# Optimization experiments

Hardware: AMD Instinct MI355X
Metric: run time of the kernel (lower is better)

Reference implementation:

```python
import jax, jax.numpy as jnp
import numpy as np

B, S, D, H = 4, 2048, 512, 8
HD = D // H  # 64


def setup_inputs() -> dict:
    key = jax.random.key(0)
    ks = jax.random.split(key, 7)
    scale = 1.0 / np.sqrt(D)
    return {
        "query": jax.random.normal(ks[0], (B, S, D), jnp.float32),
        "key": jax.random.normal(ks[1], (B, S, D), jnp.float32),
        "value": jax.random.normal(ks[2], (B, S, D), jnp.float32),
        # Only the `query` Linear and fc_out are actually used in the original forward
        "Wq": jax.random.uniform(ks[3], (D, D), jnp.float32, -scale, scale),
        "bq": jnp.zeros((D,), jnp.float32),
        "Wo": jax.random.uniform(ks[4], (D, D), jnp.float32, -scale, scale),
        "bo": jnp.zeros((D,), jnp.float32),
    }


def reference(query, key, value, Wq, bq, Wo, bo):
    # Faithful to source: Q, K, V all use the *query* projection (bug preserved)
    def proj(x):
        # [B,S,D] -> [B,H,S,HD]
        y = x @ Wq + bq
        return y.reshape(B, S, H, HD).transpose(0, 2, 1, 3)

    Q, K, V = proj(query), proj(key), proj(value)
    scores = jnp.einsum("bhqd,bhkd->bhqk", Q, K) / jnp.sqrt(jnp.float32(HD))
    attn = jax.nn.softmax(scores, axis=-1)
    x = jnp.einsum("bhqk,bhkd->bhqd", attn, V)
    x = x.transpose(0, 2, 1, 3).reshape(B, S, D)
    return x @ Wo + bo
```

## Files before the change

### kernel.cpp

```cpp
#include <hip/hip_runtime.h>
#include <math.h>

#define B_ 4
#define S_ 2048
#define D_ 512
#define H_ 8
#define HD_ 64
#define SZ_ (B_ * S_ * D_)
#define WSZ_ (D_ * D_)
#define BSH_ (B_ * S_ * H_)

#define QSCALE_ 0.18033688011112042f

typedef _Float16 v4h __attribute__((ext_vector_type(4)));
typedef _Float16 v8h __attribute__((ext_vector_type(8)));
typedef float    v4f __attribute__((ext_vector_type(4)));

__global__ __launch_bounds__(256) void wtrans_kernel(const float* __restrict__ Wq,
                                                     const float* __restrict__ Wo,
                                                     _Float16* __restrict__ Wt) {
    __shared__ float Ts[64][65];
    const float* W = blockIdx.z ? Wo : Wq;
    _Float16* dst = Wt + (size_t)blockIdx.z * WSZ_;
    const int t = threadIdx.x;
    const int k0 = blockIdx.y * 64, n0 = blockIdx.x * 64;
#pragma unroll
    for (int i = 0; i < 4; i++) {
        int c = t + i * 256;
        int kk = c >> 4, nc = (c & 15) * 4;
        float4 w = *(const float4*)&W[(size_t)(k0 + kk) * 512 + n0 + nc];
        Ts[nc + 0][kk] = w.x;
        Ts[nc + 1][kk] = w.y;
        Ts[nc + 2][kk] = w.z;
        Ts[nc + 3][kk] = w.w;
    }
    __syncthreads();
#pragma unroll
    for (int i = 0; i < 2; i++) {
        int c = t + i * 256;
        int n = c >> 3, kc = (c & 7) * 8;
        v8h p;
#pragma unroll
        for (int j = 0; j < 8; j++) p[j] = (_Float16)Ts[n][kc + j];
        *(v8h*)&dst[(size_t)(n0 + n) * 512 + k0 + kc] = p;
    }
}

__global__ __launch_bounds__(256) void proj_mfma(const float* __restrict__ q,
                                                 const float* __restrict__ k,
                                                 const float* __restrict__ v,
                                                 const _Float16* __restrict__ Wt,
                                                 const float* __restrict__ bq,
                                                 _Float16* __restrict__ Qh,
                                                 _Float16* __restrict__ Kh,
                                                 _Float16* __restrict__ VT) {
    __shared__ _Float16 As[128 * 72];
    __shared__ _Float16 Bs[128 * 72];
    const int z  = blockIdx.z;
    const float* X = (z == 0) ? q : ((z == 1) ? k : v);
    const int n0 = blockIdx.x * 128, m0 = blockIdx.y * 128;
    const int t    = threadIdx.x;
    const int lane = t & 63;
    const int w    = t >> 6;
    const int wm   = w >> 1, wn = w & 1;
    const int quad = lane >> 4, l16 = lane & 15;

    v4f acc[4][4];
#pragma unroll
    for (int mi = 0; mi < 4; mi++)
#pragma unroll
        for (int ni = 0; ni < 4; ni++) acc[mi][ni] = (v4f)0.f;

    int rr[4], cc[4];
    const float*    Ap[4];
    const _Float16* Bp[4];
#pragma unroll
    for (int i = 0; i < 4; i++) {
        int s = t + i * 256;
        rr[i] = s >> 3;
        cc[i] = (s & 7) * 8;
        Ap[i] = X + (size_t)(m0 + rr[i]) * 512 + cc[i];
        Bp[i] = Wt + (size_t)(n0 + rr[i]) * 512 + cc[i];
    }

    v4f pa[4][2];
    v8h pb[4];
#pragma unroll
    for (int i = 0; i < 4; i++) {
        pa[i][0] = *(const v4f*)(Ap[i] + 0);
        pa[i][1] = *(const v4f*)(Ap[i] + 4);
        pb[i]    = *(const v8h*)(Bp[i] + 0);
    }

    for (int k0 = 0; k0 < 512; k0 += 64) {
        v8h af4[4];
#pragma unroll
        for (int i = 0; i < 4; i++)
            af4[i] = __builtin_shufflevector(__builtin_convertvector(pa[i][0], v4h),
                                             __builtin_convertvector(pa[i][1], v4h),
                                             0, 1, 2, 3, 4, 5, 6, 7);
        __syncthreads();
#pragma unroll
        for (int i = 0; i < 4; i++) {
            *(v8h*)&As[rr[i] * 72 + cc[i]] = af4[i];
            *(v8h*)&Bs[rr[i] * 72 + cc[i]] = pb[i];
        }
        __syncthreads();

        if (k0 + 64 < 512) {
#pragma unroll
            for (int i = 0; i < 4; i++) {
                pa[i][0] = *(const v4f*)(Ap[i] + k0 + 64);
                pa[i][1] = *(const v4f*)(Ap[i] + k0 + 68);
                pb[i]    = *(const v8h*)(Bp[i] + k0 + 64);
            }
        }

#pragma unroll
        for (int ks = 0; ks < 2; ks++) {
            v8h af[4], bf[4];
#pragma unroll
            for (int mi = 0; mi < 4; mi++)
                af[mi] = *(const v8h*)&As[(wm * 64 + mi * 16 + l16) * 72 + ks * 32 + quad * 8];
#pragma unroll
            for (int ni = 0; ni < 4; ni++)
                bf[ni] = *(const v8h*)&Bs[(wn * 64 + ni * 16 + l16) * 72 + ks * 32 + quad * 8];
#pragma unroll
            for (int mi = 0; mi < 4; mi++)
#pragma unroll
                for (int ni = 0; ni < 4; ni++)
                    acc[mi][ni] = __builtin_amdgcn_mfma_f32_16x16x32_f16(af[mi], bf[ni], acc[mi][ni], 0, 0, 0);
        }
    }

    if (z < 2) {
        _Float16* Y = z ? Kh : Qh;
        const float sc = z ? 1.f : QSCALE_;
#pragma unroll
        for (int mi = 0; mi < 4; mi++) {
            int mb = m0 + wm * 64 + mi * 16 + quad * 4;
#pragma unroll
            for (int ni = 0; ni < 4; ni++) {
                int n = n0 + wn * 64 + ni * 16 + l16;
                float bj = bq[n];
#pragma unroll
                for (int r = 0; r < 4; r++)
                    Y[(size_t)(mb + r) * 512 + n] = (_Float16)((acc[mi][ni][r] + bj) * sc);
            }
        }
    } else {
#pragma unroll
        for (int mi = 0; mi < 4; mi++) {
            int tile0 = (m0 & 2047) + wm * 64;
            int pos = tile0 + (mi >> 1) * 32 + quad * 8 + (mi & 1) * 4;
            int b = m0 >> 11;
#pragma unroll
            for (int ni = 0; ni < 4; ni++) {
                int n = n0 + wn * 64 + ni * 16 + l16;
                int h = n >> 6, d = n & 63;
                float bj = bq[n];
                v4h pk;
#pragma unroll
                for (int r = 0; r < 4; r++) pk[r] = (_Float16)(acc[mi][ni][r] + bj);
                *(v4h*)&VT[(((size_t)b * H_ + h) * HD_ + d) * S_ + pos] = pk;
            }
        }
    }
}

__global__ __launch_bounds__(256) void outproj_mfma(const float* __restrict__ Op,
                                                    const float* __restrict__ lp,
                                                    const _Float16* __restrict__ Wt,
                                                    const float* __restrict__ bo,
                                                    float* __restrict__ out) {
    __shared__ _Float16 As[64 * 40];
    __shared__ _Float16 Bs[128 * 40];
    const int n0 = blockIdx.x * 128, m0 = blockIdx.y * 64;
    const int t    = threadIdx.x;
    const int lane = t & 63;
    const int w    = t >> 6;
    const int wm   = w >> 1, wn = w & 1;
    const int quad = lane >> 4, l16 = lane & 15;

    v4f acc[2][4];
#pragma unroll
    for (int mi = 0; mi < 2; mi++)
#pragma unroll
        for (int ni = 0; ni < 4; ni++) acc[mi][ni] = (v4f)0.f;

    const int ra = t >> 2,  ca = (t & 3) * 8;
    const int rb0 = t >> 2, cb0 = (t & 3) * 8;
    const int rb1 = (t + 256) >> 2, cb1 = (t & 3) * 8;
    const float* O1p = Op + (size_t)(m0 + ra) * 512 + ca;
    const float* O2p = O1p + SZ_;
    const float* lpp = lp + (size_t)(m0 + ra) * H_;
    const _Float16* B0 = Wt + (size_t)WSZ_ + (size_t)(n0 + rb0) * 512 + cb0;
    const _Float16* B1 = Wt + (size_t)WSZ_ + (size_t)(n0 + rb1) * 512 + cb1;

    v4f a0 = *(const v4f*)(O1p + 0), a1 = *(const v4f*)(O1p + 4);
    v4f c0 = *(const v4f*)(O2p + 0), c1 = *(const v4f*)(O2p + 4);
    float lv = lpp[0] + lpp[BSH_];
    v8h b0 = *(const v8h*)(B0 + 0), b1 = *(const v8h*)(B1 + 0);

    for (int k0 = 0; k0 < 512; k0 += 32) {
        float linv = __builtin_amdgcn_rcpf(lv);
        v4f sa = (a0 + c0) * linv, sb = (a1 + c1) * linv;
        v8h af0 = __builtin_shufflevector(__builtin_convertvector(sa, v4h),
                                          __builtin_convertvector(sb, v4h),
                                          0, 1, 2, 3, 4, 5, 6, 7);
        __syncthreads();
        *(v8h*)&As[ra * 40 + ca] = af0;
        *(v8h*)&Bs[rb0 * 40 + cb0] = b0;
        *(v8h*)&Bs[rb1 * 40 + cb1] = b1;
        __syncthreads();

        if (k0 + 32 < 512) {
            int kn = k0 + 32;
            int hh = (kn + ca) >> 6;
            a0 = *(const v4f*)(O1p + kn); a1 = *(const v4f*)(O1p + kn + 4);
            c0 = *(const v4f*)(O2p + kn); c1 = *(const v4f*)(O2p + kn + 4);
            lv = lpp[hh] + lpp[BSH_ + hh];
            b0 = *(const v8h*)(B0 + kn);
            b1 = *(const v8h*)(B1 + kn);
        }

        v8h af[2], bf[4];
#pragma unroll
        for (int mi = 0; mi < 2; mi++)
            af[mi] = *(const v8h*)&As[(wm * 32 + mi * 16 + l16) * 40 + quad * 8];
#pragma unroll
        for (int ni = 0; ni < 4; ni++)
            bf[ni] = *(const v8h*)&Bs[(wn * 64 + ni * 16 + l16) * 40 + quad * 8];
#pragma unroll
        for (int mi = 0; mi < 2; mi++)
#pragma unroll
            for (int ni = 0; ni < 4; ni++)
                acc[mi][ni] = __builtin_amdgcn_mfma_f32_16x16x32_f16(af[mi], bf[ni], acc[mi][ni], 0, 0, 0);
    }

#pragma unroll
    for (int mi = 0; mi < 2; mi++) {
        int mb = m0 + wm * 32 + mi * 16 + quad * 4;
#pragma unroll
        for (int ni = 0; ni < 4; ni++) {
            int n = n0 + wn * 64 + ni * 16 + l16;
            float bj = bo[n];
#pragma unroll
            for (int r = 0; r < 4; r++)
                out[(size_t)(mb + r) * 512 + n] = acc[mi][ni][r] + bj;
        }
    }
}

__global__ __launch_bounds__(256) void flash_attn_f16(const _Float16* __restrict__ Qh,
                                                      const _Float16* __restrict__ Kh,
                                                      const _Float16* __restrict__ VT,
                                                      float* __restrict__ Op,
                                                      float* __restrict__ lp) {
    __shared__ _Float16 Ks[128 * 72];
    __shared__ _Float16 Vs[64 * 136];

    const int t     = threadIdx.x;
    const int lane  = t & 63;
    const int w     = t >> 6;
    const int quad  = lane >> 4;
    const int l16   = lane & 15;
    const int q0    = blockIdx.x * 128;
    const int h     = blockIdx.y;
    const int b     = blockIdx.z >> 1;
    const int split = blockIdx.z & 1;

    const size_t base  = (size_t)b * S_ * D_ + (size_t)h * HD_;
    const size_t vbase = ((size_t)b * H_ + h) * HD_ * (size_t)S_;

    v8h qf[2][2];
#pragma unroll
    for (int nb = 0; nb < 2; nb++) {
        const _Float16* qrow = Qh + base + (size_t)(q0 + w * 32 + nb * 16 + l16) * D_;
        qf[nb][0] = *(const v8h*)(qrow + quad * 8);
        qf[nb][1] = *(const v8h*)(qrow + 32 + quad * 8);
    }

    v4f o[2][4];
#pragma unroll
    for (int nb = 0; nb < 2; nb++)
#pragma unroll
        for (int i = 0; i < 4; i++) o[nb][i] = (v4f)0.f;
    float l_lane[2] = {0.f, 0.f};

    const int kbeg = split * (S_ / 2);
    const int kend = kbeg + S_ / 2;

    v8h kv[4], vv[4];
#define LOADKV(kk)                                                             \
    do {                                                                       \
        _Pragma("unroll") for (int i = 0; i < 4; i++) {                        \
            int c = t + i * 256;                                               \
            kv[i] = *(const v8h*)(Kh + base + (size_t)((kk) + (c >> 3)) * D_ + (c & 7) * 8); \
            vv[i] = *(const v8h*)(VT + vbase + (size_t)(c >> 4) * S_ + (kk) + (c & 15) * 8); \
        }                                                                      \
    } while (0)

    LOADKV(kbeg);

    for (int kk0 = kbeg; kk0 < kend; kk0 += 128) {
        __syncthreads();
#pragma unroll
        for (int i = 0; i < 4; i++) {
            int c = t + i * 256;
            *(v8h*)&Ks[(c >> 3) * 72 + (c & 7) * 8] = kv[i];
            *(v8h*)&Vs[(c >> 4) * 136 + (c & 15) * 8] = vv[i];
        }
        __syncthreads();

        if (kk0 + 128 < kend) LOADKV(kk0 + 128);

#pragma unroll
        for (int hh = 0; hh < 2; hh++) {
            v4f sc[4][2];
#pragma unroll
            for (int mb = 0; mb < 4; mb++)
#pragma unroll
                for (int nb = 0; nb < 2; nb++) sc[mb][nb] = (v4f)0.f;
#pragma unroll
            for (int ks = 0; ks < 2; ks++) {
#pragma unroll
                for (int mb = 0; mb < 4; mb++) {
                    v8h ak = *(const v8h*)&Ks[(hh * 64 + mb * 16 + l16) * 72 + ks * 32 + quad * 8];
#pragma unroll
                    for (int nb = 0; nb < 2; nb++)
                        sc[mb][nb] = __builtin_amdgcn_mfma_f32_16x16x32_f16(ak, qf[nb][ks], sc[mb][nb], 0, 0, 0);
                }
            }

            v4h pf[4][2];
#pragma unroll
            for (int nb = 0; nb < 2; nb++) {
#pragma unroll
                for (int mb = 0; mb < 4; mb++) {
                    v4f pv;
#pragma unroll
                    for (int r = 0; r < 4; r++) pv[r] = __builtin_amdgcn_exp2f(sc[mb][nb][r]);
                    pf[mb][nb] = __builtin_convertvector(pv, v4h);
                    l_lane[nb] += (pv[0] + pv[1]) + (pv[2] + pv[3]);
                }
            }

#pragma unroll
            for (int p = 0; p < 2; p++) {
#pragma unroll
                for (int dblk = 0; dblk < 4; dblk++) {
                    v8h vf2 = *(const v8h*)&Vs[(dblk * 16 + l16) * 136 + hh * 64 + p * 32 + quad * 8];
                    v4h vlo = __builtin_shufflevector(vf2, vf2, 0, 1, 2, 3);
                    v4h vhi = __builtin_shufflevector(vf2, vf2, 4, 5, 6, 7);
#pragma unroll
                    for (int nb = 0; nb < 2; nb++) {
                        o[nb][dblk] = __builtin_amdgcn_mfma_f32_16x16x16f16(vlo, pf[2 * p][nb], o[nb][dblk], 0, 0, 0);
                        o[nb][dblk] = __builtin_amdgcn_mfma_f32_16x16x16f16(vhi, pf[2 * p + 1][nb], o[nb][dblk], 0, 0, 0);
                    }
                }
            }
        }
    }
#undef LOADKV

    float* Ops = Op + (size_t)split * SZ_;
#pragma unroll
    for (int nb = 0; nb < 2; nb++) {
        float rs = l_lane[nb];
        rs += __shfl_xor(rs, 16);
        rs += __shfl_xor(rs, 32);
        int qrow = q0 + w * 32 + nb * 16 + l16;
        if (quad == 0)
            lp[(size_t)split * BSH_ + ((size_t)b * S_ + qrow) * H_ + h] = rs;
        const size_t rbase = base + (size_t)qrow * D_;
#pragma unroll
        for (int dblk = 0; dblk < 4; dblk++)
            *(v4f*)&Ops[rbase + dblk * 16 + quad * 4] = o[nb][dblk];
    }
}

extern "C" void kernel_launch(void* const* d_in, const int* in_sizes, int n_in,
                              void* d_out, int out_size, void* d_ws, size_t ws_size,
                              hipStream_t stream) {
    const float* query = (const float*)d_in[0];
    const float* key   = (const float*)d_in[1];
    const float* value = (const float*)d_in[2];
    const float* Wq    = (const float*)d_in[3];
    const float* bq    = (const float*)d_in[4];
    const float* Wo    = (const float*)d_in[5];
    const float* bo    = (const float*)d_in[6];
    float* out = (float*)d_out;

    _Float16* ws = (_Float16*)d_ws;
    _Float16* Qh = ws;
    _Float16* Kh = ws + (size_t)SZ_;
    _Float16* VT = ws + 2 * (size_t)SZ_;
    _Float16* Wt = ws + 3 * (size_t)SZ_;
    float*    Op = (float*)(ws + 3 * (size_t)SZ_ + 2 * (size_t)WSZ_);
    float*    lp = Op + 2 * (size_t)SZ_;

    wtrans_kernel<<<dim3(8, 8, 2), 256, 0, stream>>>(Wq, Wo, Wt);
    proj_mfma<<<dim3(4, 64, 3), 256, 0, stream>>>(query, key, value, Wt, bq, Qh, Kh, VT);
    flash_attn_f16<<<dim3(S_ / 128, H_, B_ * 2), 256, 0, stream>>>(Qh, Kh, VT, Op, lp);
    outproj_mfma<<<dim3(4, 128, 1), 256, 0, stream>>>(Op, lp, Wt, bo, out);
}
```

Before: 200.6 us.

## Pre-tile weights into swizzled blocks and stream them via global_load_lds

```diff
diff --git a/kernel.cpp b/kernel.cpp
--- a/kernel.cpp
+++ b/kernel.cpp
@@ -16,38 +16,42 @@
 typedef _Float16 v8h __attribute__((ext_vector_type(8)));
 typedef float    v4f __attribute__((ext_vector_type(4)));
 
+__device__ __forceinline__ void gload16(const void* g, void* l) {
+    __builtin_amdgcn_global_load_lds((__attribute__((address_space(1))) void*)g,
+                                     (__attribute__((address_space(3))) void*)l,
+                                     16, 0, 0);
+}
+
 __global__ __launch_bounds__(256) void wtrans_kernel(const float* __restrict__ Wq,
                                                      const float* __restrict__ Wo,
                                                      _Float16* __restrict__ Wt) {
-    __shared__ float Ts[64][65];
-    const float* W = blockIdx.z ? Wo : Wq;
-    _Float16* dst = Wt + (size_t)blockIdx.z * WSZ_;
+    __shared__ float Ts[64][132];
+    const int kc = blockIdx.x, nt = blockIdx.y, mat = blockIdx.z;
+    const float* W = mat ? Wo : Wq;
+    const int k0 = kc * 64, n0 = nt * 128;
     const int t = threadIdx.x;
-    const int k0 = blockIdx.y * 64, n0 = blockIdx.x * 64;
+#pragma unroll
+    for (int i = 0; i < 8; i++) {
+        int s2 = t + i * 256;
+        int kk = s2 >> 5, nc = (s2 & 31) * 4;
+        *(float4*)&Ts[kk][nc] = *(const float4*)&W[(size_t)(k0 + kk) * 512 + n0 + nc];
+    }
+    __syncthreads();
+    _Float16* blk = Wt + (((size_t)mat * 4 + nt) * 8 + kc) * 8192;
 #pragma unroll
     for (int i = 0; i < 4; i++) {
-        int c = t + i * 256;
-        int kk = c >> 4, nc = (c & 15) * 4;
-        float4 w = *(const float4*)&W[(size_t)(k0 + kk) * 512 + n0 + nc];
-        Ts[nc + 0][kk] = w.x;
-        Ts[nc + 1][kk] = w.y;
-        Ts[nc + 2][kk] = w.z;
-        Ts[nc + 3][kk] = w.w;
-    }
-    __syncthreads();
-#pragma unroll
-    for (int i = 0; i < 2; i++) {
-        int c = t + i * 256;
-        int n = c >> 3, kc = (c & 7) * 8;
+        int s2 = t + i * 256;
+        int r = s2 >> 3, s = s2 & 7;
+        int kl = (s ^ (r & 7)) * 8;
         v8h p;
 #pragma unroll
-        for (int j = 0; j < 8; j++) p[j] = (_Float16)Ts[n][kc + j];
-        *(v8h*)&dst[(size_t)(n0 + n) * 512 + k0 + kc] = p;
+        for (int j = 0; j < 8; j++) p[j] = (_Float16)Ts[kl + j][r];
+        *(v8h*)&blk[r * 64 + s * 8] = p;
     }
 }
 
 __global__ __launch_bounds__(256) void proj_mfma(const float* __restrict__ q,
-                                                 const float* __restrict__ k,
+                                                 const float* __restrict__ kin,
                                                  const float* __restrict__ v,
                                                  const _Float16* __restrict__ Wt,
                                                  const float* __restrict__ bq,
@@ -55,15 +59,20 @@
                                                  _Float16* __restrict__ Kh,
                                                  _Float16* __restrict__ VT) {
     __shared__ _Float16 As[128 * 72];
-    __shared__ _Float16 Bs[128 * 72];
-    const int z  = blockIdx.z;
-    const float* X = (z == 0) ? q : ((z == 1) ? k : v);
-    const int n0 = blockIdx.x * 128, m0 = blockIdx.y * 128;
+    __shared__ _Float16 Bs[128 * 64];
+    const int d   = blockIdx.x;
+    const int wl  = (d & 7) * 96 + (d >> 3);
+    const int z   = wl >> 8;
+    const int rem = wl & 255;
+    const int m0  = (rem >> 2) * 128;
+    const int n_t = rem & 3, n0 = n_t * 128;
+    const float* X = (z == 0) ? q : ((z == 1) ? kin : v);
     const int t    = threadIdx.x;
     const int lane = t & 63;
     const int w    = t >> 6;
     const int wm   = w >> 1, wn = w & 1;
     const int quad = lane >> 4, l16 = lane & 15;
+    const _Float16* WtB = Wt + (size_t)n_t * 8 * 8192;
 
     v4f acc[4][4];
 #pragma unroll
@@ -72,24 +81,20 @@
         for (int ni = 0; ni < 4; ni++) acc[mi][ni] = (v4f)0.f;
 
     int rr[4], cc[4];
-    const float*    Ap[4];
-    const _Float16* Bp[4];
+    const float* Ap[4];
 #pragma unroll
     for (int i = 0; i < 4; i++) {
         int s = t + i * 256;
         rr[i] = s >> 3;
         cc[i] = (s & 7) * 8;
         Ap[i] = X + (size_t)(m0 + rr[i]) * 512 + cc[i];
-        Bp[i] = Wt + (size_t)(n0 + rr[i]) * 512 + cc[i];
     }
 
     v4f pa[4][2];
-    v8h pb[4];
 #pragma unroll
     for (int i = 0; i < 4; i++) {
         pa[i][0] = *(const v4f*)(Ap[i] + 0);
         pa[i][1] = *(const v4f*)(Ap[i] + 4);
-        pb[i]    = *(const v8h*)(Bp[i] + 0);
     }
 
     for (int k0 = 0; k0 < 512; k0 += 64) {
@@ -100,11 +105,16 @@
                                              __builtin_convertvector(pa[i][1], v4h),
                                              0, 1, 2, 3, 4, 5, 6, 7);
         __syncthreads();
-#pragma unroll
-        for (int i = 0; i < 4; i++) {
+
+        {
+            const _Float16* wsrc = WtB + (size_t)(k0 >> 6) * 8192 + w * 2048 + lane * 8;
+            _Float16* ldst = &Bs[w * 2048];
+#pragma unroll
+            for (int i = 0; i < 4; i++) gload16(wsrc + i * 512, ldst + i * 512);
+        }
+#pragma unroll
+        for (int i = 0; i < 4; i++)
             *(v8h*)&As[rr[i] * 72 + cc[i]] = af4[i];
-            *(v8h*)&Bs[rr[i] * 72 + cc[i]] = pb[i];
-        }
         __syncthreads();
 
         if (k0 + 64 < 512) {
@@ -112,7 +122,6 @@
             for (int i = 0; i < 4; i++) {
                 pa[i][0] = *(const v4f*)(Ap[i] + k0 + 64);
                 pa[i][1] = *(const v4f*)(Ap[i] + k0 + 68);
-                pb[i]    = *(const v8h*)(Bp[i] + k0 + 64);
             }
         }
 
@@ -123,8 +132,10 @@
             for (int mi = 0; mi < 4; mi++)
                 af[mi] = *(const v8h*)&As[(wm * 64 + mi * 16 + l16) * 72 + ks * 32 + quad * 8];
 #pragma unroll
-            for (int ni = 0; ni < 4; ni++)
-                bf[ni] = *(const v8h*)&Bs[(wn * 64 + ni * 16 + l16) * 72 + ks * 32 + quad * 8];
+            for (int ni = 0; ni < 4; ni++) {
+                int row = wn * 64 + ni * 16 + l16;
+                bf[ni] = *(const v8h*)&Bs[row * 64 + ((ks * 32 + quad * 8) ^ ((row & 7) * 8))];
+            }
 #pragma unroll
             for (int mi = 0; mi < 4; mi++)
 #pragma unroll
@@ -157,12 +168,12 @@
 #pragma unroll
             for (int ni = 0; ni < 4; ni++) {
                 int n = n0 + wn * 64 + ni * 16 + l16;
-                int h = n >> 6, d = n & 63;
+                int h = n >> 6, dd = n & 63;
                 float bj = bq[n];
                 v4h pk;
 #pragma unroll
                 for (int r = 0; r < 4; r++) pk[r] = (_Float16)(acc[mi][ni][r] + bj);
-                *(v4h*)&VT[(((size_t)b * H_ + h) * HD_ + d) * S_ + pos] = pk;
+                *(v4h*)&VT[(((size_t)b * H_ + h) * HD_ + dd) * S_ + pos] = pk;
             }
         }
     }
@@ -173,14 +184,18 @@
                                                     const _Float16* __restrict__ Wt,
                                                     const float* __restrict__ bo,
                                                     float* __restrict__ out) {
-    __shared__ _Float16 As[64 * 40];
-    __shared__ _Float16 Bs[128 * 40];
-    const int n0 = blockIdx.x * 128, m0 = blockIdx.y * 64;
+    __shared__ _Float16 As[64 * 72];
+    __shared__ _Float16 Bs[128 * 64];
+    const int d   = blockIdx.x;
+    const int wl  = (d & 7) * 64 + (d >> 3);
+    const int n_t = wl & 3, n0 = n_t * 128;
+    const int m0  = (wl >> 2) * 64;
     const int t    = threadIdx.x;
     const int lane = t & 63;
     const int w    = t >> 6;
     const int wm   = w >> 1, wn = w & 1;
     const int quad = lane >> 4, l16 = lane & 15;
+    const _Float16* WtB = Wt + (size_t)(4 + n_t) * 8 * 8192;
 
     v4f acc[2][4];
 #pragma unroll
@@ -188,54 +203,84 @@
 #pragma unroll
         for (int ni = 0; ni < 4; ni++) acc[mi][ni] = (v4f)0.f;
 
-    const int ra = t >> 2,  ca = (t & 3) * 8;
-    const int rb0 = t >> 2, cb0 = (t & 3) * 8;
-    const int rb1 = (t + 256) >> 2, cb1 = (t & 3) * 8;
-    const float* O1p = Op + (size_t)(m0 + ra) * 512 + ca;
-    const float* O2p = O1p + SZ_;
-    const float* lpp = lp + (size_t)(m0 + ra) * H_;
-    const _Float16* B0 = Wt + (size_t)WSZ_ + (size_t)(n0 + rb0) * 512 + cb0;
-    const _Float16* B1 = Wt + (size_t)WSZ_ + (size_t)(n0 + rb1) * 512 + cb1;
-
-    v4f a0 = *(const v4f*)(O1p + 0), a1 = *(const v4f*)(O1p + 4);
-    v4f c0 = *(const v4f*)(O2p + 0), c1 = *(const v4f*)(O2p + 4);
-    float lv = lpp[0] + lpp[BSH_];
-    v8h b0 = *(const v8h*)(B0 + 0), b1 = *(const v8h*)(B1 + 0);
-
-    for (int k0 = 0; k0 < 512; k0 += 32) {
-        float linv = __builtin_amdgcn_rcpf(lv);
-        v4f sa = (a0 + c0) * linv, sb = (a1 + c1) * linv;
-        v8h af0 = __builtin_shufflevector(__builtin_convertvector(sa, v4h),
-                                          __builtin_convertvector(sb, v4h),
-                                          0, 1, 2, 3, 4, 5, 6, 7);
-        __syncthreads();
-        *(v8h*)&As[ra * 40 + ca] = af0;
-        *(v8h*)&Bs[rb0 * 40 + cb0] = b0;
-        *(v8h*)&Bs[rb1 * 40 + cb1] = b1;
-        __syncthreads();
-
-        if (k0 + 32 < 512) {
-            int kn = k0 + 32;
-            int hh = (kn + ca) >> 6;
-            a0 = *(const v4f*)(O1p + kn); a1 = *(const v4f*)(O1p + kn + 4);
-            c0 = *(const v4f*)(O2p + kn); c1 = *(const v4f*)(O2p + kn + 4);
-            lv = lpp[hh] + lpp[BSH_ + hh];
-            b0 = *(const v8h*)(B0 + kn);
-            b1 = *(const v8h*)(B1 + kn);
-        }
-
-        v8h af[2], bf[4];
-#pragma unroll
-        for (int mi = 0; mi < 2; mi++)
-            af[mi] = *(const v8h*)&As[(wm * 32 + mi * 16 + l16) * 40 + quad * 8];
-#pragma unroll
-        for (int ni = 0; ni < 4; ni++)
-            bf[ni] = *(const v8h*)&Bs[(wn * 64 + ni * 16 + l16) * 40 + quad * 8];
-#pragma unroll
-        for (int mi = 0; mi < 2; mi++)
-#pragma unroll
-            for (int ni = 0; ni < 4; ni++)
-                acc[mi][ni] = __builtin_amdgcn_mfma_f32_16x16x32_f16(af[mi], bf[ni], acc[mi][ni], 0, 0, 0);
+    int rw[2], cw[2];
+    const float* O1p[2];
+    const float* O2p[2];
+    const float* lpp[2];
+#pragma unroll
+    for (int i = 0; i < 2; i++) {
+        int s2 = t + i * 256;
+        rw[i] = s2 >> 3;
+        cw[i] = (s2 & 7) * 8;
+        O1p[i] = Op + (size_t)(m0 + rw[i]) * 512 + cw[i];
+        O2p[i] = O1p[i] + SZ_;
+        lpp[i] = lp + (size_t)(m0 + rw[i]) * H_;
+    }
+
+    v4f pa0[2], pa1[2], pc0[2], pc1[2];
+    float lvv[2];
+#pragma unroll
+    for (int i = 0; i < 2; i++) {
+        pa0[i] = *(const v4f*)(O1p[i] + 0);
+        pa1[i] = *(const v4f*)(O1p[i] + 4);
+        pc0[i] = *(const v4f*)(O2p[i] + 0);
+        pc1[i] = *(const v4f*)(O2p[i] + 4);
+        lvv[i] = lpp[i][0] + lpp[i][BSH_];
+    }
+
+    for (int k0 = 0; k0 < 512; k0 += 64) {
+        v8h af16[2];
+#pragma unroll
+        for (int i = 0; i < 2; i++) {
+            float linv = __builtin_amdgcn_rcpf(lvv[i]);
+            v4f sa = (pa0[i] + pc0[i]) * linv;
+            v4f sb = (pa1[i] + pc1[i]) * linv;
+            af16[i] = __builtin_shufflevector(__builtin_convertvector(sa, v4h),
+                                              __builtin_convertvector(sb, v4h),
+                                              0, 1, 2, 3, 4, 5, 6, 7);
+        }
+        __syncthreads();
+
+        {
+            const _Float16* wsrc = WtB + (size_t)(k0 >> 6) * 8192 + w * 2048 + lane * 8;
+            _Float16* ldst = &Bs[w * 2048];
+#pragma unroll
+            for (int i = 0; i < 4; i++) gload16(wsrc + i * 512, ldst + i * 512);
+        }
+#pragma unroll
+        for (int i = 0; i < 2; i++)
+            *(v8h*)&As[rw[i] * 72 + cw[i]] = af16[i];
+        __syncthreads();
+
+        if (k0 + 64 < 512) {
+            int kn = k0 + 64, hh = kn >> 6;
+#pragma unroll
+            for (int i = 0; i < 2; i++) {
+                pa0[i] = *(const v4f*)(O1p[i] + kn);
+                pa1[i] = *(const v4f*)(O1p[i] + kn + 4);
+                pc0[i] = *(const v4f*)(O2p[i] + kn);
+                pc1[i] = *(const v4f*)(O2p[i] + kn + 4);
+                lvv[i] = lpp[i][hh] + lpp[i][BSH_ + hh];
+            }
+        }
+
+#pragma unroll
+        for (int ks = 0; ks < 2; ks++) {
+            v8h af[2], bf[4];
+#pragma unroll
+            for (int mi = 0; mi < 2; mi++)
+                af[mi] = *(const v8h*)&As[(wm * 32 + mi * 16 + l16) * 72 + ks * 32 + quad * 8];
+#pragma unroll
+            for (int ni = 0; ni < 4; ni++) {
+                int row = wn * 64 + ni * 16 + l16;
+                bf[ni] = *(const v8h*)&Bs[row * 64 + ((ks * 32 + quad * 8) ^ ((row & 7) * 8))];
+            }
+#pragma unroll
+            for (int mi = 0; mi < 2; mi++)
+#pragma unroll
+                for (int ni = 0; ni < 4; ni++)
+                    acc[mi][ni] = __builtin_amdgcn_mfma_f32_16x16x32_f16(af[mi], bf[ni], acc[mi][ni], 0, 0, 0);
+        }
     }
 
 #pragma unroll
@@ -400,8 +445,8 @@
     float*    Op = (float*)(ws + 3 * (size_t)SZ_ + 2 * (size_t)WSZ_);
     float*    lp = Op + 2 * (size_t)SZ_;
 
-    wtrans_kernel<<<dim3(8, 8, 2), 256, 0, stream>>>(Wq, Wo, Wt);
-    proj_mfma<<<dim3(4, 64, 3), 256, 0, stream>>>(query, key, value, Wt, bq, Qh, Kh, VT);
+    wtrans_kernel<<<dim3(8, 4, 2), 256, 0, stream>>>(Wq, Wo, Wt);
+    proj_mfma<<<dim3(768), 256, 0, stream>>>(query, key, value, Wt, bq, Qh, Kh, VT);
     flash_attn_f16<<<dim3(S_ / 128, H_, B_ * 2), 256, 0, stream>>>(Qh, Kh, VT, Op, lp);
-    outproj_mfma<<<dim3(4, 128, 1), 256, 0, stream>>>(Op, lp, Wt, bo, out);
-}
+    outproj_mfma<<<dim3(512), 256, 0, stream>>>(Op, lp, Wt, bo, out);
+}
```

After: 197.3 us. About the same (-1.7%).

## Keep full weight slice in LDS and stream activations directly from global

Applied to the files above, without the earlier changes.

```diff
diff --git a/kernel.cpp b/kernel.cpp
--- a/kernel.cpp
+++ b/kernel.cpp
@@ -16,153 +16,131 @@
 typedef _Float16 v8h __attribute__((ext_vector_type(8)));
 typedef float    v4f __attribute__((ext_vector_type(4)));
 
+__device__ __forceinline__ void gload16(const void* g, void* l) {
+    __builtin_amdgcn_global_load_lds((__attribute__((address_space(1))) void*)g,
+                                     (__attribute__((address_space(3))) void*)l,
+                                     16, 0, 0);
+}
+
+__device__ __forceinline__ v8h pack8(v4f a, v4f b) {
+    return __builtin_shufflevector(__builtin_convertvector(a, v4h),
+                                   __builtin_convertvector(b, v4h),
+                                   0, 1, 2, 3, 4, 5, 6, 7);
+}
+
 __global__ __launch_bounds__(256) void wtrans_kernel(const float* __restrict__ Wq,
                                                      const float* __restrict__ Wo,
                                                      _Float16* __restrict__ Wt) {
-    __shared__ float Ts[64][65];
-    const float* W = blockIdx.z ? Wo : Wq;
-    _Float16* dst = Wt + (size_t)blockIdx.z * WSZ_;
+    __shared__ float Ts[64][68];
+    const int kc = blockIdx.x, nt = blockIdx.y, mat = blockIdx.z;
+    const float* W = mat ? Wo : Wq;
+    const int k0 = kc * 64, n0 = nt * 64;
     const int t = threadIdx.x;
-    const int k0 = blockIdx.y * 64, n0 = blockIdx.x * 64;
 #pragma unroll
     for (int i = 0; i < 4; i++) {
-        int c = t + i * 256;
-        int kk = c >> 4, nc = (c & 15) * 4;
-        float4 w = *(const float4*)&W[(size_t)(k0 + kk) * 512 + n0 + nc];
-        Ts[nc + 0][kk] = w.x;
-        Ts[nc + 1][kk] = w.y;
-        Ts[nc + 2][kk] = w.z;
-        Ts[nc + 3][kk] = w.w;
+        int s2 = t + i * 256;
+        int kk = s2 >> 4, nc = (s2 & 15) * 4;
+        *(float4*)&Ts[kk][nc] = *(const float4*)&W[(size_t)(k0 + kk) * 512 + n0 + nc];
     }
     __syncthreads();
+    _Float16* blk = Wt + (((size_t)mat * 8 + nt) * 8 + kc) * 4096;
 #pragma unroll
     for (int i = 0; i < 2; i++) {
-        int c = t + i * 256;
-        int n = c >> 3, kc = (c & 7) * 8;
+        int s2 = t + i * 256;
+        int r = s2 >> 3, s = s2 & 7;
+        int kl = (s ^ (r & 7)) * 8;
         v8h p;
 #pragma unroll
-        for (int j = 0; j < 8; j++) p[j] = (_Float16)Ts[n][kc + j];
-        *(v8h*)&dst[(size_t)(n0 + n) * 512 + k0 + kc] = p;
+        for (int j = 0; j < 8; j++) p[j] = (_Float16)Ts[kl + j][r];
+        *(v8h*)&blk[r * 64 + s * 8] = p;
     }
 }
 
 __global__ __launch_bounds__(256) void proj_mfma(const float* __restrict__ q,
-                                                 const float* __restrict__ k,
+                                                 const float* __restrict__ kin,
                                                  const float* __restrict__ v,
                                                  const _Float16* __restrict__ Wt,
                                                  const float* __restrict__ bq,
                                                  _Float16* __restrict__ Qh,
                                                  _Float16* __restrict__ Kh,
                                                  _Float16* __restrict__ VT) {
-    __shared__ _Float16 As[128 * 72];
-    __shared__ _Float16 Bs[128 * 72];
-    const int z  = blockIdx.z;
-    const float* X = (z == 0) ? q : ((z == 1) ? k : v);
-    const int n0 = blockIdx.x * 128, m0 = blockIdx.y * 128;
-    const int t    = threadIdx.x;
-    const int lane = t & 63;
-    const int w    = t >> 6;
-    const int wm   = w >> 1, wn = w & 1;
+    __shared__ __align__(16) _Float16 Bs[32768];
+    const int dblk = blockIdx.x;
+    const int xcd = dblk & 7, ii = dblk >> 3;
+    const int nt = ii & 7;
+    const int g  = ((ii >> 3) << 3) | xcd;
+    const int z  = g >> 5;
+    const int m0 = (g & 31) * 256;
+    const float* X = (z == 0) ? q : ((z == 1) ? kin : v);
+    const int t = threadIdx.x;
+    const int lane = t & 63, w = t >> 6;
     const int quad = lane >> 4, l16 = lane & 15;
 
-    v4f acc[4][4];
-#pragma unroll
-    for (int mi = 0; mi < 4; mi++)
-#pragma unroll
-        for (int ni = 0; ni < 4; ni++) acc[mi][ni] = (v4f)0.f;
-
-    int rr[4], cc[4];
-    const float*    Ap[4];
-    const _Float16* Bp[4];
-#pragma unroll
-    for (int i = 0; i < 4; i++) {
-        int s = t + i * 256;
-        rr[i] = s >> 3;
-        cc[i] = (s & 7) * 8;
-        Ap[i] = X + (size_t)(m0 + rr[i]) * 512 + cc[i];
-        Bp[i] = Wt + (size_t)(n0 + rr[i]) * 512 + cc[i];
-    }
-
-    v4f pa[4][2];
-    v8h pb[4];
-#pragma unroll
-    for (int i = 0; i < 4; i++) {
-        pa[i][0] = *(const v4f*)(Ap[i] + 0);
-        pa[i][1] = *(const v4f*)(Ap[i] + 4);
-        pb[i]    = *(const v8h*)(Bp[i] + 0);
-    }
-
-    for (int k0 = 0; k0 < 512; k0 += 64) {
-        v8h af4[4];
-#pragma unroll
-        for (int i = 0; i < 4; i++)
-            af4[i] = __builtin_shufflevector(__builtin_convertvector(pa[i][0], v4h),
-                                             __builtin_convertvector(pa[i][1], v4h),
-                                             0, 1, 2, 3, 4, 5, 6, 7);
-        __syncthreads();
-#pragma unroll
-        for (int i = 0; i < 4; i++) {
-            *(v8h*)&As[rr[i] * 72 + cc[i]] = af4[i];
-            *(v8h*)&Bs[rr[i] * 72 + cc[i]] = pb[i];
-        }
-        __syncthreads();
-
-        if (k0 + 64 < 512) {
-#pragma unroll
-            for (int i = 0; i < 4; i++) {
-                pa[i][0] = *(const v4f*)(Ap[i] + k0 + 64);
-                pa[i][1] = *(const v4f*)(Ap[i] + k0 + 68);
-                pb[i]    = *(const v8h*)(Bp[i] + k0 + 64);
-            }
-        }
-
-#pragma unroll
-        for (int ks = 0; ks < 2; ks++) {
-            v8h af[4], bf[4];
-#pragma unroll
-            for (int mi = 0; mi < 4; mi++)
-                af[mi] = *(const v8h*)&As[(wm * 64 + mi * 16 + l16) * 72 + ks * 32 + quad * 8];
-#pragma unroll
-            for (int ni = 0; ni < 4; ni++)
-                bf[ni] = *(const v8h*)&Bs[(wn * 64 + ni * 16 + l16) * 72 + ks * 32 + quad * 8];
-#pragma unroll
-            for (int mi = 0; mi < 4; mi++)
-#pragma unroll
-                for (int ni = 0; ni < 4; ni++)
-                    acc[mi][ni] = __builtin_amdgcn_mfma_f32_16x16x32_f16(af[mi], bf[ni], acc[mi][ni], 0, 0, 0);
-        }
-    }
-
-    if (z < 2) {
-        _Float16* Y = z ? Kh : Qh;
-        const float sc = z ? 1.f : QSCALE_;
-#pragma unroll
-        for (int mi = 0; mi < 4; mi++) {
-            int mb = m0 + wm * 64 + mi * 16 + quad * 4;
-#pragma unroll
-            for (int ni = 0; ni < 4; ni++) {
-                int n = n0 + wn * 64 + ni * 16 + l16;
-                float bj = bq[n];
-#pragma unroll
-                for (int r = 0; r < 4; r++)
-                    Y[(size_t)(mb + r) * 512 + n] = (_Float16)((acc[mi][ni][r] + bj) * sc);
-            }
-        }
-    } else {
-#pragma unroll
-        for (int mi = 0; mi < 4; mi++) {
-            int tile0 = (m0 & 2047) + wm * 64;
-            int pos = tile0 + (mi >> 1) * 32 + quad * 8 + (mi & 1) * 4;
-            int b = m0 >> 11;
-#pragma unroll
-            for (int ni = 0; ni < 4; ni++) {
-                int n = n0 + wn * 64 + ni * 16 + l16;
-                int h = n >> 6, d = n & 63;
-                float bj = bq[n];
-                v4h pk;
-#pragma unroll
-                for (int r = 0; r < 4; r++) pk[r] = (_Float16)(acc[mi][ni][r] + bj);
-                *(v4h*)&VT[(((size_t)b * H_ + h) * HD_ + d) * S_ + pos] = pk;
+    const _Float16* psrc = Wt + (size_t)nt * 32768 + ((size_t)w * 64 + lane) * 8;
+    _Float16* pdst = &Bs[(size_t)w * 512];
+#pragma unroll
+    for (int j = 0; j < 16; j++)
+        gload16(psrc + j * 2048, pdst + j * 2048);
+    __syncthreads();
+
+    for (int pass = 0; pass < 2; ++pass) {
+        const int r0 = m0 + pass * 128 + w * 32;
+        const float* A0 = X + (size_t)(r0 + l16) * 512 + quad * 8;
+        const float* A1 = A0 + 16 * 512;
+
+        v4f acc[2][4];
+#pragma unroll
+        for (int mi = 0; mi < 2; mi++)
+#pragma unroll
+            for (int ni = 0; ni < 4; ni++) acc[mi][ni] = (v4f)0.f;
+
+#pragma unroll
+        for (int kc = 0; kc < 8; ++kc) {
+#pragma unroll
+            for (int ks = 0; ks < 2; ++ks) {
+                const int ko = kc * 64 + ks * 32;
+                v8h af0 = pack8(*(const v4f*)(A0 + ko), *(const v4f*)(A0 + ko + 4));
+                v8h af1 = pack8(*(const v4f*)(A1 + ko), *(const v4f*)(A1 + ko + 4));
+                const int sx = ks * 32 + quad * 8;
+#pragma unroll
+                for (int ni = 0; ni < 4; ++ni) {
+                    const int rb = ni * 16 + l16;
+                    v8h bf = *(const v8h*)&Bs[kc * 4096 + rb * 64 + (sx ^ ((rb & 7) * 8))];
+                    acc[0][ni] = __builtin_amdgcn_mfma_f32_16x16x32_f16(af0, bf, acc[0][ni], 0, 0, 0);
+                    acc[1][ni] = __builtin_amdgcn_mfma_f32_16x16x32_f16(af1, bf, acc[1][ni], 0, 0, 0);
+                }
+            }
+        }
+
+        if (z < 2) {
+            _Float16* Y = z ? Kh : Qh;
+            const float sc = z ? 1.f : QSCALE_;
+#pragma unroll
+            for (int mi = 0; mi < 2; mi++) {
+                int mb = r0 + mi * 16 + quad * 4;
+#pragma unroll
+                for (int ni = 0; ni < 4; ni++) {
+                    int n = nt * 64 + ni * 16 + l16;
+                    float bj = bq[n];
+#pragma unroll
+                    for (int r = 0; r < 4; r++)
+                        Y[(size_t)(mb + r) * 512 + n] = (_Float16)((acc[mi][ni][r] + bj) * sc);
+                }
+            }
+        } else {
+            const int b = r0 >> 11;
+#pragma unroll
+            for (int mi = 0; mi < 2; mi++) {
+                int pos = (r0 & 2047) + quad * 8 + mi * 4;
+#pragma unroll
+                for (int ni = 0; ni < 4; ni++) {
+                    int n = nt * 64 + ni * 16 + l16;
+                    float bj = bq[n];
+                    v4h pk;
+#pragma unroll
+                    for (int r = 0; r < 4; r++) pk[r] = (_Float16)(acc[mi][ni][r] + bj);
+                    *(v4h*)&VT[(((size_t)b * H_ + nt) * HD_ + ni * 16 + l16) * S_ + pos] = pk;
+                }
             }
         }
     }
@@ -173,81 +151,78 @@
                                                     const _Float16* __restrict__ Wt,
                                                     const float* __restrict__ bo,
                                                     float* __restrict__ out) {
-    __shared__ _Float16 As[64 * 40];
-    __shared__ _Float16 Bs[128 * 40];
-    const int n0 = blockIdx.x * 128, m0 = blockIdx.y * 64;
-    const int t    = threadIdx.x;
-    const int lane = t & 63;
-    const int w    = t >> 6;
-    const int wm   = w >> 1, wn = w & 1;
+    __shared__ __align__(16) _Float16 Bs[32768];
+    const int dblk = blockIdx.x;
+    const int xcd = dblk & 7, ii = dblk >> 3;
+    const int nt = ii & 7;
+    const int mc = ((ii >> 3) << 3) | xcd;
+    const int m0 = mc * 256;
+    const int t = threadIdx.x;
+    const int lane = t & 63, w = t >> 6;
     const int quad = lane >> 4, l16 = lane & 15;
 
-    v4f acc[2][4];
-#pragma unroll
-    for (int mi = 0; mi < 2; mi++)
-#pragma unroll
-        for (int ni = 0; ni < 4; ni++) acc[mi][ni] = (v4f)0.f;
-
-    const int ra = t >> 2,  ca = (t & 3) * 8;
-    const int rb0 = t >> 2, cb0 = (t & 3) * 8;
-    const int rb1 = (t + 256) >> 2, cb1 = (t & 3) * 8;
-    const float* O1p = Op + (size_t)(m0 + ra) * 512 + ca;
-    const float* O2p = O1p + SZ_;
-    const float* lpp = lp + (size_t)(m0 + ra) * H_;
-    const _Float16* B0 = Wt + (size_t)WSZ_ + (size_t)(n0 + rb0) * 512 + cb0;
-    const _Float16* B1 = Wt + (size_t)WSZ_ + (size_t)(n0 + rb1) * 512 + cb1;
-
-    v4f a0 = *(const v4f*)(O1p + 0), a1 = *(const v4f*)(O1p + 4);
-    v4f c0 = *(const v4f*)(O2p + 0), c1 = *(const v4f*)(O2p + 4);
-    float lv = lpp[0] + lpp[BSH_];
-    v8h b0 = *(const v8h*)(B0 + 0), b1 = *(const v8h*)(B1 + 0);
-
-    for (int k0 = 0; k0 < 512; k0 += 32) {
-        float linv = __builtin_amdgcn_rcpf(lv);
-        v4f sa = (a0 + c0) * linv, sb = (a1 + c1) * linv;
-        v8h af0 = __builtin_shufflevector(__builtin_convertvector(sa, v4h),
-                                          __builtin_convertvector(sb, v4h),
-                                          0, 1, 2, 3, 4, 5, 6, 7);
-        __syncthreads();
-        *(v8h*)&As[ra * 40 + ca] = af0;
-        *(v8h*)&Bs[rb0 * 40 + cb0] = b0;
-        *(v8h*)&Bs[rb1 * 40 + cb1] = b1;
-        __syncthreads();
-
-        if (k0 + 32 < 512) {
-            int kn = k0 + 32;
-            int hh = (kn + ca) >> 6;
-            a0 = *(const v4f*)(O1p + kn); a1 = *(const v4f*)(O1p + kn + 4);
-            c0 = *(const v4f*)(O2p + kn); c1 = *(const v4f*)(O2p + kn + 4);
-            lv = lpp[hh] + lpp[BSH_ + hh];
-            b0 = *(const v8h*)(B0 + kn);
-            b1 = *(const v8h*)(B1 + kn);
-        }
-
-        v8h af[2], bf[4];
+    const _Float16* psrc = Wt + (size_t)(8 + nt) * 32768 + ((size_t)w * 64 + lane) * 8;
+    _Float16* pdst = &Bs[(size_t)w * 512];
+#pragma unroll
+    for (int j = 0; j < 16; j++)
+        gload16(psrc + j * 2048, pdst + j * 2048);
+    __syncthreads();
+
+    for (int pass = 0; pass < 2; ++pass) {
+        const int r0 = m0 + pass * 128 + w * 32;
+        const float* P0 = Op + (size_t)(r0 + l16) * 512 + quad * 8;
+        const float* P1 = P0 + 16 * 512;
+        const float* Q0 = P0 + SZ_;
+        const float* Q1 = P1 + SZ_;
+        const float* lp0 = lp + (size_t)(r0 + l16) * 8;
+        const float* lp1 = lp0 + 16 * 8;
+
+        float linv0[8], linv1[8];
+#pragma unroll
+        for (int kc = 0; kc < 8; kc++) {
+            linv0[kc] = __builtin_amdgcn_rcpf(lp0[kc] + lp0[BSH_ + kc]);
+            linv1[kc] = __builtin_amdgcn_rcpf(lp1[kc] + lp1[BSH_ + kc]);
+        }
+
+        v4f acc[2][4];
 #pragma unroll
         for (int mi = 0; mi < 2; mi++)
-            af[mi] = *(const v8h*)&As[(wm * 32 + mi * 16 + l16) * 40 + quad * 8];
-#pragma unroll
-        for (int ni = 0; ni < 4; ni++)
-            bf[ni] = *(const v8h*)&Bs[(wn * 64 + ni * 16 + l16) * 40 + quad * 8];
-#pragma unroll
-        for (int mi = 0; mi < 2; mi++)
-#pragma unroll
-            for (int ni = 0; ni < 4; ni++)
-                acc[mi][ni] = __builtin_amdgcn_mfma_f32_16x16x32_f16(af[mi], bf[ni], acc[mi][ni], 0, 0, 0);
-    }
-
-#pragma unroll
-    for (int mi = 0; mi < 2; mi++) {
-        int mb = m0 + wm * 32 + mi * 16 + quad * 4;
-#pragma unroll
-        for (int ni = 0; ni < 4; ni++) {
-            int n = n0 + wn * 64 + ni * 16 + l16;
-            float bj = bo[n];
-#pragma unroll
-            for (int r = 0; r < 4; r++)
-                out[(size_t)(mb + r) * 512 + n] = acc[mi][ni][r] + bj;
+#pragma unroll
+            for (int ni = 0; ni < 4; ni++) acc[mi][ni] = (v4f)0.f;
+
+#pragma unroll
+        for (int kc = 0; kc < 8; ++kc) {
+#pragma unroll
+            for (int ks = 0; ks < 2; ++ks) {
+                const int ko = kc * 64 + ks * 32;
+                v4f s00 = (*(const v4f*)(P0 + ko) + *(const v4f*)(Q0 + ko)) * linv0[kc];
+                v4f s01 = (*(const v4f*)(P0 + ko + 4) + *(const v4f*)(Q0 + ko + 4)) * linv0[kc];
+                v4f s10 = (*(const v4f*)(P1 + ko) + *(const v4f*)(Q1 + ko)) * linv1[kc];
+                v4f s11 = (*(const v4f*)(P1 + ko + 4) + *(const v4f*)(Q1 + ko + 4)) * linv1[kc];
+                v8h af0 = pack8(s00, s01);
+                v8h af1 = pack8(s10, s11);
+                const int sx = ks * 32 + quad * 8;
+#pragma unroll
+                for (int ni = 0; ni < 4; ++ni) {
+                    const int rb = ni * 16 + l16;
+                    v8h bf = *(const v8h*)&Bs[kc * 4096 + rb * 64 + (sx ^ ((rb & 7) * 8))];
+                    acc[0][ni] = __builtin_amdgcn_mfma_f32_16x16x32_f16(af0, bf, acc[0][ni], 0, 0, 0);
+                    acc[1][ni] = __builtin_amdgcn_mfma_f32_16x16x32_f16(af1, bf, acc[1][ni], 0, 0, 0);
+                }
+            }
+        }
+
+#pragma unroll
+        for (int mi = 0; mi < 2; mi++) {
+            int mb = r0 + mi * 16 + quad * 4;
+#pragma unroll
+            for (int ni = 0; ni < 4; ni++) {
+                int n = nt * 64 + ni * 16 + l16;
+                float bj = bo[n];
+#pragma unroll
+                for (int r = 0; r < 4; r++)
+                    out[(size_t)(mb + r) * 512 + n] = acc[mi][ni][r] + bj;
+            }
         }
     }
 }
@@ -401,7 +376,7 @@
     float*    lp = Op + 2 * (size_t)SZ_;
 
     wtrans_kernel<<<dim3(8, 8, 2), 256, 0, stream>>>(Wq, Wo, Wt);
-    proj_mfma<<<dim3(4, 64, 3), 256, 0, stream>>>(query, key, value, Wt, bq, Qh, Kh, VT);
+    proj_mfma<<<dim3(768), 256, 0, stream>>>(query, key, value, Wt, bq, Qh, Kh, VT);
     flash_attn_f16<<<dim3(S_ / 128, H_, B_ * 2), 256, 0, stream>>>(Qh, Kh, VT, Op, lp);
-    outproj_mfma<<<dim3(4, 128, 1), 256, 0, stream>>>(Op, lp, Wt, bo, out);
-}
+    outproj_mfma<<<dim3(256), 256, 0, stream>>>(Op, lp, Wt, bo, out);
+}
```

New measurement: 282.5 us. 40.9% more time.
